# Kernel tuning notes

Measured on AMD Instinct MI355X. Metric: run time of the kernel, lower is better.

## Reference

```python
import jax, jax.numpy as jnp
import numpy as np

D_MODEL = 2048
D_HEAD = 128
NUM_HEADS = 16
D_KV_LATENT = 512
BATCH = 2
SEQ = 2048


def setup_inputs() -> dict:
    key = jax.random.key(0)
    ks = jax.random.split(key, 6)
    s = 0.02
    return {
        "x": jax.random.normal(ks[0], (BATCH, SEQ, D_MODEL), jnp.float32),
        "Wd": jax.random.normal(ks[1], (D_KV_LATENT, D_MODEL), jnp.float32) * s,
        "Wuk": jax.random.normal(ks[2], (NUM_HEADS * D_HEAD, D_KV_LATENT), jnp.float32) * s,
        "Wuv": jax.random.normal(ks[3], (NUM_HEADS * D_HEAD, D_KV_LATENT), jnp.float32) * s,
        "Wq": jax.random.normal(ks[4], (NUM_HEADS * D_HEAD, D_MODEL), jnp.float32) * s,
        "Wo": jax.random.normal(ks[5], (D_MODEL, NUM_HEADS * D_HEAD), jnp.float32) * s,
        "use_cache": 1,
    }


def _mla_cache_path(x, Wd, Wuk, Wuv, Wq, Wo):
    # Weight-absorbed MLA prefill from an empty cache (total_seq_len == seq_len).
    b, s, dm = x.shape
    h, dh, c = NUM_HEADS, D_HEAD, D_KV_LATENT
    # latents = downsample(x): [b, s, c]
    latents = jnp.einsum("bsm,cm->bsc", x, Wd)
    # absorbed weights: q_uk [h, dm, c], out_uv [h, dm, c]
    q_uk = jnp.einsum("hdm,hdc->hmc", Wq.reshape(h, dh, dm), Wuk.reshape(h, dh, c))
    out_uv = jnp.einsum("mhd,hdc->hmc", Wo.reshape(dm, h, dh), Wuv.reshape(h, dh, c))
    # query_part: [b, h, s, c]
    query_part = jnp.einsum("bsm,hmc->bhsc", x, q_uk)
    # value_part: [b, h, s, dm]
    value_part = jnp.einsum("hmc,btc->bhtm", out_uv, latents)
    # scores over latent dim: [b, h, s, s]
    scores = jnp.einsum("bhsc,btc->bhst", query_part, latents) / np.sqrt(dh).astype(np.float32)
    causal = jnp.triu(jnp.ones((s, s), dtype=bool), k=1)
    scores = jnp.where(causal, -jnp.inf, scores)
    attn = jax.nn.softmax(scores, axis=-1)
    # output already in model dim; sum contributions over heads
    out = jnp.einsum("bhst,bhtm->bsm", attn, value_part)
    return out


def reference(x, Wd, Wuk, Wuv, Wq, Wo, use_cache):
    # use_cache is a static Python int (1 -> weight-absorbed cache path)
    return _mla_cache_path(x, Wd, Wuk, Wuv, Wq, Wo)
```

## Files before the change

### kernel.cpp

```cpp
#include <hip/hip_runtime.h>
#include <hip/hip_bf16.h>

typedef __attribute__((ext_vector_type(8))) short short8x;
typedef __attribute__((ext_vector_type(4))) float f32x4;

__device__ __forceinline__ ushort f2bf(float f){
  union { __hip_bfloat16 b; ushort u; } cvt;
  cvt.b = __float2bfloat16(f);
  return cvt.u;
}

__global__ __launch_bounds__(256) void cvt_kernel(const float* __restrict__ in, ushort* __restrict__ out,
                                                  long n, float scale){
  long i = ((long)blockIdx.x * 256 + threadIdx.x) * 4;
  if (i >= n) return;
  float4 v = *(const float4*)(in + i);
  ushort4 o;
  o.x = f2bf(v.x * scale); o.y = f2bf(v.y * scale); o.z = f2bf(v.z * scale); o.w = f2bf(v.w * scale);
  *(ushort4*)(out + i) = o;
}

template<int OUTBF>
__global__ __launch_bounds__(256, 3)
void gemm_bt(const ushort* __restrict__ A, const ushort* __restrict__ BT, void* __restrict__ Cv,
             int M, int N, int K, int lda, int ldb, int ldc,
             long aZ, long bZ, long cZ, float scale)
{
  __shared__ __align__(16) ushort As[2][128 * 32];
  __shared__ __align__(16) ushort Bs[2][128 * 32];
  const int z = blockIdx.z;
  const ushort* Ab = A + (long)z * aZ;
  const ushort* Bb = BT + (long)z * bZ;
  const int tid = threadIdx.x, lane = tid & 63, w = tid >> 6;
  const int wm = w >> 1, wn = w & 1;
  const int lq = lane & 15, q4 = lane >> 4;

  int lin = blockIdx.x + gridDim.x * blockIdx.y;
  const int cpx = (gridDim.x * gridDim.y) >> 3;
  lin = (lin & 7) * cpx + (lin >> 3);
  const int bx = lin % gridDim.x, by = lin / gridDim.x;

  const long arow = (long)by * 128, brow = (long)bx * 128;
  const int lr = lane >> 2, lc = (lane & 3) * 8;

  const f32x4 z4 = {0.f, 0.f, 0.f, 0.f};
  f32x4 acc[4][4];
#pragma unroll
  for (int i = 0; i < 4; i++)
#pragma unroll
    for (int j = 0; j < 4; j++) acc[i][j] = z4;

  auto stage = [&](int buf, int k0){
#pragma unroll
    for (int is = 0; is < 2; ++is){
      const int rb = is * 64 + w * 16;
      const ushort* ga = Ab + (arow + rb + lr) * (long)lda + k0 + lc;
      const ushort* gb = Bb + (brow + rb + lr) * (long)ldb + k0 + lc;
      __builtin_amdgcn_global_load_lds((const __attribute__((address_space(1))) void*)ga,
                                       (__attribute__((address_space(3))) void*)&As[buf][rb * 32], 16, 0, 0);
      __builtin_amdgcn_global_load_lds((const __attribute__((address_space(1))) void*)gb,
                                       (__attribute__((address_space(3))) void*)&Bs[buf][rb * 32], 16, 0, 0);
    }
  };

  const int nk = K >> 5;
  stage(0, 0);
  for (int kt = 0; kt < nk; ++kt){
    __syncthreads();
    if (kt + 1 < nk) stage((kt + 1) & 1, (kt + 1) * 32);
    const int buf = kt & 1;
    short8x a[4], b[4];
#pragma unroll
    for (int i = 0; i < 4; i++){
      a[i] = *(const short8x*)&As[buf][(wm * 64 + i * 16 + lq) * 32 + q4 * 8];
      b[i] = *(const short8x*)&Bs[buf][(wn * 64 + i * 16 + lq) * 32 + q4 * 8];
    }
#pragma unroll
    for (int i = 0; i < 4; i++)
#pragma unroll
      for (int j = 0; j < 4; j++)
        acc[i][j] = __builtin_amdgcn_mfma_f32_16x16x32_bf16(a[i], b[j], acc[i][j], 0, 0, 0);
  }

  const long crowb = arow + wm * 64;
  const long ccolb = brow + wn * 64;
#pragma unroll
  for (int i = 0; i < 4; i++)
#pragma unroll
    for (int j = 0; j < 4; j++)
#pragma unroll
      for (int r = 0; r < 4; r++){
        const long row = crowb + i * 16 + q4 * 4 + r;
        const long col = ccolb + j * 16 + lq;
        const float v = acc[i][j][r] * scale;
        if (OUTBF) ((ushort*)Cv)[(long)z * cZ + row * ldc + col] = f2bf(v);
        else       ((float*)Cv)[(long)z * cZ + row * ldc + col] = v;
      }
}

__global__ __launch_bounds__(256, 1)
void flash12_kernel(const ushort* __restrict__ q, const ushort* __restrict__ k,
                    const ushort* __restrict__ vT, ushort* __restrict__ attnO)
{
  __shared__ __align__(16) ushort Kb[2][64 * 128];
  __shared__ __align__(16) ushort Vb[2][128 * 64];
  __shared__ __align__(16) ushort Pl[4][2][16][64];

  const int tid = threadIdx.x, lane = tid & 63, w = tid >> 6;
  const int lq = lane & 15, q4 = lane >> 4;

  const int i = blockIdx.x;
  const int pr = i >> 8;
  const int ii = i & 255;
  const int xcd = ii & 7;
  const int bh = xcd * 4 + ((ii >> 3) & 3);
  const int j = ii >> 5;
  const int strip = pr ? j : (15 - j);
  const int b = bh & 1, h = bh >> 1;

  const int nt = 2 * (strip + 1);
  const int wdiag = strip * 2 + (w >> 1);
  const int moff = (w & 1) * 32;

  const ushort* kb_ = k + (long)b * 2048 * 2048 + h * 128;
  const ushort* vb_ = vT + (long)h * 128 * 4096 + (long)b * 2048;

  const int krow0 = w * 4 + (lane >> 4);
  const int kg = (lane & 15) ^ (krow0 & 7);
  const ushort* kbase = kb_ + (long)krow0 * 2048 + kg * 8;
  const int kofs0 = w * 512;

  const int drow0 = w * 8 + (lane >> 3);
  const int vg = (lane & 7) ^ (drow0 & 7);
  const ushort* vbase = vb_ + (long)drow0 * 4096 + vg * 8;
  const int vofs0 = w * 512;

  auto stage = [&](int buf, int tt){
    const ushort* kp = kbase + (long)tt * 64 * 2048;
    const ushort* vp = vbase + (long)tt * 64;
#pragma unroll
    for (int is = 0; is < 4; ++is){
      __builtin_amdgcn_global_load_lds((const __attribute__((address_space(1))) void*)(kp + (long)is * 16 * 2048),
          (__attribute__((address_space(3))) void*)&Kb[buf][kofs0 + is * 2048], 16, 0, 0);
      __builtin_amdgcn_global_load_lds((const __attribute__((address_space(1))) void*)(vp + (long)is * 32 * 4096),
          (__attribute__((address_space(3))) void*)&Vb[buf][vofs0 + is * 2048], 16, 0, 0);
    }
  };

  const f32x4 z4 = {0.f, 0.f, 0.f, 0.f};

  const int qrow0 = strip * 128 + w * 32;
  const long qgbase = (long)b * 2048 + qrow0;

  short8x qf[2][4];
#pragma unroll
  for (int si = 0; si < 2; si++){
    const ushort* qp = q + (qgbase + si * 16 + lq) * 2560 + h * 128 + q4 * 8;
#pragma unroll
    for (int ks = 0; ks < 4; ks++) qf[si][ks] = *(const short8x*)(qp + ks * 32);
  }

  f32x4 oacc[8][2];
#pragma unroll
  for (int dt = 0; dt < 8; dt++){ oacc[dt][0] = z4; oacc[dt][1] = z4; }
  float dsum[2] = {0.f, 0.f};

  const int prx = lq & 7;

  stage(0, 0);
  stage(1, 1);

#pragma unroll 1
  for (int tt = 0; tt < nt; ++tt){
    if (tt == nt - 1) asm volatile("s_waitcnt vmcnt(0)" ::: "memory");
    else              asm volatile("s_waitcnt vmcnt(8)" ::: "memory");
    __syncthreads();
    const int cur = tt & 1;

    if (tt <= wdiag){
      const bool diag = (tt == wdiag);
#pragma unroll
      for (int ti = 0; ti < 4; ++ti){
        const int r = ti * 16 + lq;
        const int rb = r * 128;
        const int rx = r & 7;
        const short8x a0 = *(const short8x*)&Kb[cur][rb + (((q4) ^ rx) * 8)];
        const short8x a1 = *(const short8x*)&Kb[cur][rb + (((4 + q4) ^ rx) * 8)];
        const short8x a2 = *(const short8x*)&Kb[cur][rb + (((8 + q4) ^ rx) * 8)];
        const short8x a3 = *(const short8x*)&Kb[cur][rb + (((12 + q4) ^ rx) * 8)];
        const int cG = (ti * 2 + (q4 >> 1)) ^ prx;
        const int pco = cG * 8 + (q4 & 1) * 4;
#pragma unroll
        for (int si = 0; si < 2; ++si){
          f32x4 st = __builtin_amdgcn_mfma_f32_16x16x32_bf16(a0, qf[si][0], z4, 0, 0, 0);
          st = __builtin_amdgcn_mfma_f32_16x16x32_bf16(a1, qf[si][1], st, 0, 0, 0);
          st = __builtin_amdgcn_mfma_f32_16x16x32_bf16(a2, qf[si][2], st, 0, 0, 0);
          st = __builtin_amdgcn_mfma_f32_16x16x32_bf16(a3, qf[si][3], st, 0, 0, 0);
          ushort4 pb;
#pragma unroll
          for (int r4 = 0; r4 < 4; ++r4){
            const int tl = ti * 16 + q4 * 4 + r4;
            float p = exp2f(st[r4]);
            if (diag && tl > moff + si * 16 + lq) p = 0.f;
            dsum[si] += p;
            ((ushort*)&pb)[r4] = f2bf(p);
          }
          *(ushort4*)&Pl[w][si][lq][pco] = pb;
        }
      }
      asm volatile("s_waitcnt lgkmcnt(0)" ::: "memory");
      __builtin_amdgcn_sched_barrier(0);
      const short8x pf00 = *(const short8x*)&Pl[w][0][lq][(q4 ^ prx) * 8];
      const short8x pf01 = *(const short8x*)&Pl[w][0][lq][((4 + q4) ^ prx) * 8];
      const short8x pf10 = *(const short8x*)&Pl[w][1][lq][(q4 ^ prx) * 8];
      const short8x pf11 = *(const short8x*)&Pl[w][1][lq][((4 + q4) ^ prx) * 8];
      __builtin_amdgcn_sched_barrier(0);
#pragma unroll
      for (int dt = 0; dt < 8; ++dt){
        const int r = dt * 16 + lq;
        const int rb = r * 64;
        const int rx = lq & 7;
        const short8x av0 = *(const short8x*)&Vb[cur][rb + (((q4) ^ rx) * 8)];
        const short8x av1 = *(const short8x*)&Vb[cur][rb + (((4 + q4) ^ rx) * 8)];
        oacc[dt][0] = __builtin_amdgcn_mfma_f32_16x16x32_bf16(av0, pf00, oacc[dt][0], 0, 0, 0);
        oacc[dt][0] = __builtin_amdgcn_mfma_f32_16x16x32_bf16(av1, pf01, oacc[dt][0], 0, 0, 0);
        oacc[dt][1] = __builtin_amdgcn_mfma_f32_16x16x32_bf16(av0, pf10, oacc[dt][1], 0, 0, 0);
        oacc[dt][1] = __builtin_amdgcn_mfma_f32_16x16x32_bf16(av1, pf11, oacc[dt][1], 0, 0, 0);
      }
    }
    __syncthreads();
    if (tt + 2 < nt) stage(cur, tt + 2);
  }

  float inv[2];
#pragma unroll
  for (int si = 0; si < 2; ++si){
    float d = dsum[si];
    d += __shfl_xor(d, 16);
    d += __shfl_xor(d, 32);
    inv[si] = 1.f / d;
  }

#pragma unroll
  for (int dt = 0; dt < 8; dt++)
#pragma unroll
    for (int si = 0; si < 2; si++){
      ushort4 o;
      o.x = f2bf(oacc[dt][si][0] * inv[si]);
      o.y = f2bf(oacc[dt][si][1] * inv[si]);
      o.z = f2bf(oacc[dt][si][2] * inv[si]);
      o.w = f2bf(oacc[dt][si][3] * inv[si]);
      *(ushort4*)(attnO + (qgbase + si * 16 + lq) * 2048 + h * 128 + dt * 16 + q4 * 4) = o;
    }
}

extern "C" void kernel_launch(void* const* d_in, const int* in_sizes, int n_in,
                              void* d_out, int out_size, void* d_ws, size_t ws_size,
                              hipStream_t stream)
{
  const float* x   = (const float*)d_in[0];
  const float* Wd  = (const float*)d_in[1];
  const float* Wuk = (const float*)d_in[2];
  const float* Wuv = (const float*)d_in[3];
  const float* Wq  = (const float*)d_in[4];
  const float* Wo  = (const float*)d_in[5];
  float* out = (float*)d_out;
  ushort* ws = (ushort*)d_ws;

  ushort* xb    = ws + 0L;
  ushort* wqdb  = ws + 8388608L;
  ushort* wob   = ws + 13631488L;
  ushort* wukb  = ws + 17825792L;
  ushort* wuvb  = ws + 18874368L;
  ushort* qlat  = ws + 19922944L;
  ushort* kb    = ws + 30408704L;
  ushort* vTb   = ws + 38797312L;
  ushort* attnO = ws + 47185920L;

  const float QSCL = 0.12751744800f;

  cvt_kernel<<<8192, 256, 0, stream>>>(x,   xb,            8388608L, 1.0f);
  cvt_kernel<<<4096, 256, 0, stream>>>(Wq,  wqdb,          4194304L, QSCL);
  cvt_kernel<<<1024, 256, 0, stream>>>(Wd,  wqdb + 4194304L, 1048576L, 1.0f);
  cvt_kernel<<<4096, 256, 0, stream>>>(Wo,  wob,           4194304L, 1.0f);
  cvt_kernel<<<1024, 256, 0, stream>>>(Wuk, wukb,          1048576L, 1.0f);
  cvt_kernel<<<1024, 256, 0, stream>>>(Wuv, wuvb,          1048576L, 1.0f);

  gemm_bt<1><<<dim3(20, 32, 1), 256, 0, stream>>>(xb, wqdb, qlat, 4096, 2560, 2048,
      2048, 2048, 2560, 0L, 0L, 0L, 1.0f);
  gemm_bt<1><<<dim3(16, 32, 1), 256, 0, stream>>>(qlat + 2048, wukb, kb, 4096, 2048, 512,
      2560, 512, 2048, 0L, 0L, 0L, 1.0f);
  gemm_bt<1><<<dim3(32, 16, 1), 256, 0, stream>>>(wuvb, qlat + 2048, vTb, 2048, 4096, 512,
      512, 2560, 4096, 0L, 0L, 0L, 1.0f);
  flash12_kernel<<<512, 256, 0, stream>>>(qlat, kb, vTb, attnO);
  gemm_bt<0><<<dim3(16, 32, 1), 256, 0, stream>>>(attnO, wob, out, 4096, 2048, 2048,
      2048, 2048, 2048, 0L, 0L, 0L, 1.0f);
}
```

Before: 237.8 us.

## Replace 128x128 GEMM with 256x256 tile, swizzled LDS, two-stage prefetch

Rewrites the bf16 GEMM to use 256x256 output tiles with 512 threads, a K step of 64, XOR-swizzled LDS layout, and two buffers prefetched ahead with explicit vmcnt waits and wave priority hints. The aim is to raise operand reuse per LDS load and hide global-load latency behind MFMA work. All four projection GEMMs switch to it. The larger tiles cut the block count below the CU count and use a large LDS footprint, which can leave compute units idle, especially for the K=512 GEMMs.

```diff
diff --git a/kernel.cpp b/kernel.cpp
--- a/kernel.cpp
+++ b/kernel.cpp
@@ -21,71 +21,103 @@
 }
 
 template<int OUTBF>
-__global__ __launch_bounds__(256, 3)
-void gemm_bt(const ushort* __restrict__ A, const ushort* __restrict__ BT, void* __restrict__ Cv,
-             int M, int N, int K, int lda, int ldb, int ldc,
-             long aZ, long bZ, long cZ, float scale)
+__global__ __launch_bounds__(512, 1)
+void gemm256(const ushort* __restrict__ A, const ushort* __restrict__ BT, void* __restrict__ Cv,
+             int K, int lda, int ldb, int ldc, float scale)
 {
-  __shared__ __align__(16) ushort As[2][128 * 32];
-  __shared__ __align__(16) ushort Bs[2][128 * 32];
-  const int z = blockIdx.z;
-  const ushort* Ab = A + (long)z * aZ;
-  const ushort* Bb = BT + (long)z * bZ;
+  __shared__ __align__(16) ushort As[2][256 * 64];
+  __shared__ __align__(16) ushort Bs[2][256 * 64];
   const int tid = threadIdx.x, lane = tid & 63, w = tid >> 6;
-  const int wm = w >> 1, wn = w & 1;
   const int lq = lane & 15, q4 = lane >> 4;
+  const int wm = w >> 2, wn = w & 3;
 
   int lin = blockIdx.x + gridDim.x * blockIdx.y;
   const int cpx = (gridDim.x * gridDim.y) >> 3;
   lin = (lin & 7) * cpx + (lin >> 3);
   const int bx = lin % gridDim.x, by = lin / gridDim.x;
-
-  const long arow = (long)by * 128, brow = (long)bx * 128;
-  const int lr = lane >> 2, lc = (lane & 3) * 8;
+  const long arow = (long)by * 256, brow = (long)bx * 256;
+
+  const int srow = tid >> 3;
+  const int sg = (tid & 7) ^ (srow & 7);
+  const ushort* Abase = A + (arow + srow) * (long)lda + sg * 8;
+  const ushort* Bbase = BT + (brow + srow) * (long)ldb + sg * 8;
+  const int dof = w * 512;
+
+  auto stage = [&](int buf, int kt){
+    const long kc = (long)kt * 64;
+#pragma unroll
+    for (int s = 0; s < 4; ++s){
+      __builtin_amdgcn_global_load_lds(
+          (const __attribute__((address_space(1))) void*)(Abase + (long)(s * 64) * lda + kc),
+          (__attribute__((address_space(3))) void*)&As[buf][s * 4096 + dof], 16, 0, 0);
+      __builtin_amdgcn_global_load_lds(
+          (const __attribute__((address_space(1))) void*)(Bbase + (long)(s * 64) * ldb + kc),
+          (__attribute__((address_space(3))) void*)&Bs[buf][s * 4096 + dof], 16, 0, 0);
+    }
+  };
 
   const f32x4 z4 = {0.f, 0.f, 0.f, 0.f};
-  f32x4 acc[4][4];
-#pragma unroll
-  for (int i = 0; i < 4; i++)
+  f32x4 acc[8][4];
+#pragma unroll
+  for (int i = 0; i < 8; i++)
 #pragma unroll
     for (int j = 0; j < 4; j++) acc[i][j] = z4;
 
-  auto stage = [&](int buf, int k0){
-#pragma unroll
-    for (int is = 0; is < 2; ++is){
-      const int rb = is * 64 + w * 16;
-      const ushort* ga = Ab + (arow + rb + lr) * (long)lda + k0 + lc;
-      const ushort* gb = Bb + (brow + rb + lr) * (long)ldb + k0 + lc;
-      __builtin_amdgcn_global_load_lds((const __attribute__((address_space(1))) void*)ga,
-                                       (__attribute__((address_space(3))) void*)&As[buf][rb * 32], 16, 0, 0);
-      __builtin_amdgcn_global_load_lds((const __attribute__((address_space(1))) void*)gb,
-                                       (__attribute__((address_space(3))) void*)&Bs[buf][rb * 32], 16, 0, 0);
-    }
-  };
-
-  const int nk = K >> 5;
+  const int rx = lq & 7;
+  const int arb = wm * 128;
+  const int brb = wn * 64;
+
+  const int nk = K >> 6;
   stage(0, 0);
+  stage(1, 1);
+
+#pragma unroll 1
   for (int kt = 0; kt < nk; ++kt){
+    if (kt == nk - 1) asm volatile("s_waitcnt vmcnt(0)" ::: "memory");
+    else              asm volatile("s_waitcnt vmcnt(8)" ::: "memory");
     __syncthreads();
-    if (kt + 1 < nk) stage((kt + 1) & 1, (kt + 1) * 32);
     const int buf = kt & 1;
-    short8x a[4], b[4];
-#pragma unroll
-    for (int i = 0; i < 4; i++){
-      a[i] = *(const short8x*)&As[buf][(wm * 64 + i * 16 + lq) * 32 + q4 * 8];
-      b[i] = *(const short8x*)&Bs[buf][(wn * 64 + i * 16 + lq) * 32 + q4 * 8];
-    }
-#pragma unroll
-    for (int i = 0; i < 4; i++)
-#pragma unroll
-      for (int j = 0; j < 4; j++)
-        acc[i][j] = __builtin_amdgcn_mfma_f32_16x16x32_bf16(a[i], b[j], acc[i][j], 0, 0, 0);
+
+#pragma unroll
+    for (int q = 0; q < 4; ++q){
+      const int mi = q & 1, nj = q >> 1;
+      short8x af[4][2], bf[2][2];
+#pragma unroll
+      for (int i2 = 0; i2 < 4; ++i2){
+        const int R = arb + (mi * 4 + i2) * 16 + lq;
+#pragma unroll
+        for (int kk = 0; kk < 2; ++kk)
+          af[i2][kk] = *(const short8x*)&As[buf][R * 64 + (((kk * 4 + q4) ^ rx) * 8)];
+      }
+#pragma unroll
+      for (int j2 = 0; j2 < 2; ++j2){
+        const int R = brb + (nj * 2 + j2) * 16 + lq;
+#pragma unroll
+        for (int kk = 0; kk < 2; ++kk)
+          bf[j2][kk] = *(const short8x*)&Bs[buf][R * 64 + (((kk * 4 + q4) ^ rx) * 8)];
+      }
+      asm volatile("s_waitcnt lgkmcnt(0)" ::: "memory");
+      __builtin_amdgcn_sched_barrier(0);
+      __builtin_amdgcn_s_setprio(1);
+#pragma unroll
+      for (int kk = 0; kk < 2; ++kk)
+#pragma unroll
+        for (int i2 = 0; i2 < 4; ++i2)
+#pragma unroll
+          for (int j2 = 0; j2 < 2; ++j2)
+            acc[mi * 4 + i2][nj * 2 + j2] =
+                __builtin_amdgcn_mfma_f32_16x16x32_bf16(af[i2][kk], bf[j2][kk],
+                                                        acc[mi * 4 + i2][nj * 2 + j2], 0, 0, 0);
+      __builtin_amdgcn_s_setprio(0);
+    }
+    __syncthreads();
+    if (kt + 2 < nk) stage(buf, kt + 2);
   }
 
-  const long crowb = arow + wm * 64;
+  const long crowb = arow + wm * 128;
   const long ccolb = brow + wn * 64;
 #pragma unroll
-  for (int i = 0; i < 4; i++)
+  for (int i = 0; i < 8; i++)
 #pragma unroll
     for (int j = 0; j < 4; j++)
 #pragma unroll
@@ -93,8 +125,8 @@
         const long row = crowb + i * 16 + q4 * 4 + r;
         const long col = ccolb + j * 16 + lq;
         const float v = acc[i][j][r] * scale;
-        if (OUTBF) ((ushort*)Cv)[(long)z * cZ + row * ldc + col] = f2bf(v);
-        else       ((float*)Cv)[(long)z * cZ + row * ldc + col] = v;
+        if (OUTBF) ((ushort*)Cv)[row * ldc + col] = f2bf(v);
+        else       ((float*)Cv)[row * ldc + col] = v;
       }
 }
 
@@ -183,11 +215,11 @@
       for (int ti = 0; ti < 4; ++ti){
         const int r = ti * 16 + lq;
         const int rb = r * 128;
-        const int rx = r & 7;
-        const short8x a0 = *(const short8x*)&Kb[cur][rb + (((q4) ^ rx) * 8)];
-        const short8x a1 = *(const short8x*)&Kb[cur][rb + (((4 + q4) ^ rx) * 8)];
-        const short8x a2 = *(const short8x*)&Kb[cur][rb + (((8 + q4) ^ rx) * 8)];
-        const short8x a3 = *(const short8x*)&Kb[cur][rb + (((12 + q4) ^ rx) * 8)];
+        const int rxk = r & 7;
+        const short8x a0 = *(const short8x*)&Kb[cur][rb + (((q4) ^ rxk) * 8)];
+        const short8x a1 = *(const short8x*)&Kb[cur][rb + (((4 + q4) ^ rxk) * 8)];
+        const short8x a2 = *(const short8x*)&Kb[cur][rb + (((8 + q4) ^ rxk) * 8)];
+        const short8x a3 = *(const short8x*)&Kb[cur][rb + (((12 + q4) ^ rxk) * 8)];
         const int cG = (ti * 2 + (q4 >> 1)) ^ prx;
         const int pco = cG * 8 + (q4 & 1) * 4;
 #pragma unroll
@@ -219,9 +251,9 @@
       for (int dt = 0; dt < 8; ++dt){
         const int r = dt * 16 + lq;
         const int rb = r * 64;
-        const int rx = lq & 7;
-        const short8x av0 = *(const short8x*)&Vb[cur][rb + (((q4) ^ rx) * 8)];
-        const short8x av1 = *(const short8x*)&Vb[cur][rb + (((4 + q4) ^ rx) * 8)];
+        const int rxv = lq & 7;
+        const short8x av0 = *(const short8x*)&Vb[cur][rb + (((q4) ^ rxv) * 8)];
+        const short8x av1 = *(const short8x*)&Vb[cur][rb + (((4 + q4) ^ rxv) * 8)];
         oacc[dt][0] = __builtin_amdgcn_mfma_f32_16x16x32_bf16(av0, pf00, oacc[dt][0], 0, 0, 0);
         oacc[dt][0] = __builtin_amdgcn_mfma_f32_16x16x32_bf16(av1, pf01, oacc[dt][0], 0, 0, 0);
         oacc[dt][1] = __builtin_amdgcn_mfma_f32_16x16x32_bf16(av0, pf10, oacc[dt][1], 0, 0, 0);
@@ -286,13 +318,9 @@
   cvt_kernel<<<1024, 256, 0, stream>>>(Wuk, wukb,          1048576L, 1.0f);
   cvt_kernel<<<1024, 256, 0, stream>>>(Wuv, wuvb,          1048576L, 1.0f);
 
-  gemm_bt<1><<<dim3(20, 32, 1), 256, 0, stream>>>(xb, wqdb, qlat, 4096, 2560, 2048,
-      2048, 2048, 2560, 0L, 0L, 0L, 1.0f);
-  gemm_bt<1><<<dim3(16, 32, 1), 256, 0, stream>>>(qlat + 2048, wukb, kb, 4096, 2048, 512,
-      2560, 512, 2048, 0L, 0L, 0L, 1.0f);
-  gemm_bt<1><<<dim3(32, 16, 1), 256, 0, stream>>>(wuvb, qlat + 2048, vTb, 2048, 4096, 512,
-      512, 2560, 4096, 0L, 0L, 0L, 1.0f);
+  gemm256<1><<<dim3(10, 16), 512, 0, stream>>>(xb, wqdb, qlat, 2048, 2048, 2048, 2560, 1.0f);
+  gemm256<1><<<dim3(8, 16), 512, 0, stream>>>(qlat + 2048, wukb, kb, 512, 2560, 512, 2048, 1.0f);
+  gemm256<1><<<dim3(16, 8), 512, 0, stream>>>(wuvb, qlat + 2048, vTb, 512, 512, 2560, 4096, 1.0f);
   flash12_kernel<<<512, 256, 0, stream>>>(qlat, kb, vTb, attnO);
-  gemm_bt<0><<<dim3(16, 32, 1), 256, 0, stream>>>(attnO, wob, out, 4096, 2048, 2048,
-      2048, 2048, 2048, 0L, 0L, 0L, 1.0f);
-}
+  gemm256<0><<<dim3(8, 16), 512, 0, stream>>>(attnO, wob, out, 2048, 2048, 2048, 2048, 1.0f);
+}
```

New measurement: 295.7 us. 1.24x slower.

## Halve flash attention tile sizes to raise occupancy and block count

Applied to the files above, without the earlier changes.

The attention kernel now processes 64-row query strips with 16 rows per wave and 32-key tiles, instead of 128-row strips and 64-key tiles. This cuts LDS and registers per block so four blocks can share a CU, and launches 1024 blocks with a reworked strip and XCD mapping for causal load balance. In exchange, each block issues twice as many tile iterations and barriers, K/V reuse per load is lower, and the V and P LDS layouts drop their swizzle, which may add bank conflicts.

```diff
diff --git a/kernel.cpp b/kernel.cpp
--- a/kernel.cpp
+++ b/kernel.cpp
@@ -98,29 +98,27 @@
       }
 }
 
-__global__ __launch_bounds__(256, 1)
-void flash12_kernel(const ushort* __restrict__ q, const ushort* __restrict__ k,
+__global__ __launch_bounds__(256, 4)
+void flash13_kernel(const ushort* __restrict__ q, const ushort* __restrict__ k,
                     const ushort* __restrict__ vT, ushort* __restrict__ attnO)
 {
-  __shared__ __align__(16) ushort Kb[2][64 * 128];
-  __shared__ __align__(16) ushort Vb[2][128 * 64];
-  __shared__ __align__(16) ushort Pl[4][2][16][64];
+  __shared__ __align__(16) ushort Kb[2][32 * 128];
+  __shared__ __align__(16) ushort Vb[2][128 * 32];
+  __shared__ __align__(16) ushort Pl[4][16][40];
 
   const int tid = threadIdx.x, lane = tid & 63, w = tid >> 6;
   const int lq = lane & 15, q4 = lane >> 4;
 
-  const int i = blockIdx.x;
-  const int pr = i >> 8;
-  const int ii = i & 255;
-  const int xcd = ii & 7;
-  const int bh = xcd * 4 + ((ii >> 3) & 3);
-  const int j = ii >> 5;
-  const int strip = pr ? j : (15 - j);
+  const int blk = blockIdx.x;
+  const int bh = (blk & 7) * 4 + ((blk >> 3) & 3);
+  const int g = blk >> 5;
+  const int u = (g & 7) * 4 + (g >> 3);
+  const int strip = (u & 1) ? (u >> 1) : (31 - (u >> 1));
   const int b = bh & 1, h = bh >> 1;
 
-  const int nt = 2 * (strip + 1);
+  const int nt = 2 * strip + 2;
   const int wdiag = strip * 2 + (w >> 1);
-  const int moff = (w & 1) * 32;
+  const int moff = (w & 1) * 16;
 
   const ushort* kb_ = k + (long)b * 2048 * 2048 + h * 128;
   const ushort* vb_ = vT + (long)h * 128 * 4096 + (long)b * 2048;
@@ -128,44 +126,38 @@
   const int krow0 = w * 4 + (lane >> 4);
   const int kg = (lane & 15) ^ (krow0 & 7);
   const ushort* kbase = kb_ + (long)krow0 * 2048 + kg * 8;
-  const int kofs0 = w * 512;
-
-  const int drow0 = w * 8 + (lane >> 3);
-  const int vg = (lane & 7) ^ (drow0 & 7);
-  const ushort* vbase = vb_ + (long)drow0 * 4096 + vg * 8;
-  const int vofs0 = w * 512;
+
+  const int drow0 = w * 16 + (lane >> 2);
+  const ushort* vbase = vb_ + (long)drow0 * 4096 + (lane & 3) * 8;
 
   auto stage = [&](int buf, int tt){
-    const ushort* kp = kbase + (long)tt * 64 * 2048;
-    const ushort* vp = vbase + (long)tt * 64;
-#pragma unroll
-    for (int is = 0; is < 4; ++is){
+    const ushort* kp = kbase + (long)tt * 32 * 2048;
+    const ushort* vp = vbase + (long)tt * 32;
+#pragma unroll
+    for (int is = 0; is < 2; ++is){
       __builtin_amdgcn_global_load_lds((const __attribute__((address_space(1))) void*)(kp + (long)is * 16 * 2048),
-          (__attribute__((address_space(3))) void*)&Kb[buf][kofs0 + is * 2048], 16, 0, 0);
-      __builtin_amdgcn_global_load_lds((const __attribute__((address_space(1))) void*)(vp + (long)is * 32 * 4096),
-          (__attribute__((address_space(3))) void*)&Vb[buf][vofs0 + is * 2048], 16, 0, 0);
+          (__attribute__((address_space(3))) void*)&Kb[buf][w * 512 + is * 2048], 16, 0, 0);
+      __builtin_amdgcn_global_load_lds((const __attribute__((address_space(1))) void*)(vp + (long)is * 64 * 4096),
+          (__attribute__((address_space(3))) void*)&Vb[buf][w * 512 + is * 2048], 16, 0, 0);
     }
   };
 
   const f32x4 z4 = {0.f, 0.f, 0.f, 0.f};
 
-  const int qrow0 = strip * 128 + w * 32;
+  const int qrow0 = strip * 64 + w * 16;
   const long qgbase = (long)b * 2048 + qrow0;
 
-  short8x qf[2][4];
-#pragma unroll
-  for (int si = 0; si < 2; si++){
-    const ushort* qp = q + (qgbase + si * 16 + lq) * 2560 + h * 128 + q4 * 8;
-#pragma unroll
-    for (int ks = 0; ks < 4; ks++) qf[si][ks] = *(const short8x*)(qp + ks * 32);
-  }
-
-  f32x4 oacc[8][2];
-#pragma unroll
-  for (int dt = 0; dt < 8; dt++){ oacc[dt][0] = z4; oacc[dt][1] = z4; }
-  float dsum[2] = {0.f, 0.f};
-
-  const int prx = lq & 7;
+  short8x qf[4];
+  {
+    const ushort* qp = q + (qgbase + lq) * 2560 + h * 128 + q4 * 8;
+#pragma unroll
+    for (int ks = 0; ks < 4; ks++) qf[ks] = *(const short8x*)(qp + ks * 32);
+  }
+
+  f32x4 oacc[8];
+#pragma unroll
+  for (int dt = 0; dt < 8; dt++) oacc[dt] = z4;
+  float dsum = 0.f;
 
   stage(0, 0);
   stage(1, 1);
@@ -173,85 +165,63 @@
 #pragma unroll 1
   for (int tt = 0; tt < nt; ++tt){
     if (tt == nt - 1) asm volatile("s_waitcnt vmcnt(0)" ::: "memory");
-    else              asm volatile("s_waitcnt vmcnt(8)" ::: "memory");
+    else              asm volatile("s_waitcnt vmcnt(4)" ::: "memory");
     __syncthreads();
     const int cur = tt & 1;
 
     if (tt <= wdiag){
       const bool diag = (tt == wdiag);
 #pragma unroll
-      for (int ti = 0; ti < 4; ++ti){
+      for (int ti = 0; ti < 2; ++ti){
         const int r = ti * 16 + lq;
         const int rb = r * 128;
-        const int rx = r & 7;
+        const int rx = lq & 7;
         const short8x a0 = *(const short8x*)&Kb[cur][rb + (((q4) ^ rx) * 8)];
         const short8x a1 = *(const short8x*)&Kb[cur][rb + (((4 + q4) ^ rx) * 8)];
         const short8x a2 = *(const short8x*)&Kb[cur][rb + (((8 + q4) ^ rx) * 8)];
         const short8x a3 = *(const short8x*)&Kb[cur][rb + (((12 + q4) ^ rx) * 8)];
-        const int cG = (ti * 2 + (q4 >> 1)) ^ prx;
-        const int pco = cG * 8 + (q4 & 1) * 4;
-#pragma unroll
-        for (int si = 0; si < 2; ++si){
-          f32x4 st = __builtin_amdgcn_mfma_f32_16x16x32_bf16(a0, qf[si][0], z4, 0, 0, 0);
-          st = __builtin_amdgcn_mfma_f32_16x16x32_bf16(a1, qf[si][1], st, 0, 0, 0);
-          st = __builtin_amdgcn_mfma_f32_16x16x32_bf16(a2, qf[si][2], st, 0, 0, 0);
-          st = __builtin_amdgcn_mfma_f32_16x16x32_bf16(a3, qf[si][3], st, 0, 0, 0);
-          ushort4 pb;
-#pragma unroll
-          for (int r4 = 0; r4 < 4; ++r4){
-            const int tl = ti * 16 + q4 * 4 + r4;
-            float p = exp2f(st[r4]);
-            if (diag && tl > moff + si * 16 + lq) p = 0.f;
-            dsum[si] += p;
-            ((ushort*)&pb)[r4] = f2bf(p);
-          }
-          *(ushort4*)&Pl[w][si][lq][pco] = pb;
+        f32x4 st = __builtin_amdgcn_mfma_f32_16x16x32_bf16(a0, qf[0], z4, 0, 0, 0);
+        st = __builtin_amdgcn_mfma_f32_16x16x32_bf16(a1, qf[1], st, 0, 0, 0);
+        st = __builtin_amdgcn_mfma_f32_16x16x32_bf16(a2, qf[2], st, 0, 0, 0);
+        st = __builtin_amdgcn_mfma_f32_16x16x32_bf16(a3, qf[3], st, 0, 0, 0);
+        ushort4 pb;
+#pragma unroll
+        for (int r4 = 0; r4 < 4; ++r4){
+          const int tl = ti * 16 + q4 * 4 + r4;
+          float p = exp2f(st[r4]);
+          if (diag && tl > moff + lq) p = 0.f;
+          dsum += p;
+          ((ushort*)&pb)[r4] = f2bf(p);
         }
+        *(ushort4*)&Pl[w][lq][ti * 16 + q4 * 4] = pb;
       }
       asm volatile("s_waitcnt lgkmcnt(0)" ::: "memory");
       __builtin_amdgcn_sched_barrier(0);
-      const short8x pf00 = *(const short8x*)&Pl[w][0][lq][(q4 ^ prx) * 8];
-      const short8x pf01 = *(const short8x*)&Pl[w][0][lq][((4 + q4) ^ prx) * 8];
-      const short8x pf10 = *(const short8x*)&Pl[w][1][lq][(q4 ^ prx) * 8];
-      const short8x pf11 = *(const short8x*)&Pl[w][1][lq][((4 + q4) ^ prx) * 8];
+      const short8x pf = *(const short8x*)&Pl[w][lq][q4 * 8];
       __builtin_amdgcn_sched_barrier(0);
 #pragma unroll
       for (int dt = 0; dt < 8; ++dt){
-        const int r = dt * 16 + lq;
-        const int rb = r * 64;
-        const int rx = lq & 7;
-        const short8x av0 = *(const short8x*)&Vb[cur][rb + (((q4) ^ rx) * 8)];
-        const short8x av1 = *(const short8x*)&Vb[cur][rb + (((4 + q4) ^ rx) * 8)];
-        oacc[dt][0] = __builtin_amdgcn_mfma_f32_16x16x32_bf16(av0, pf00, oacc[dt][0], 0, 0, 0);
-        oacc[dt][0] = __builtin_amdgcn_mfma_f32_16x16x32_bf16(av1, pf01, oacc[dt][0], 0, 0, 0);
-        oacc[dt][1] = __builtin_amdgcn_mfma_f32_16x16x32_bf16(av0, pf10, oacc[dt][1], 0, 0, 0);
-        oacc[dt][1] = __builtin_amdgcn_mfma_f32_16x16x32_bf16(av1, pf11, oacc[dt][1], 0, 0, 0);
+        const short8x av = *(const short8x*)&Vb[cur][(dt * 16 + lq) * 32 + q4 * 8];
+        oacc[dt] = __builtin_amdgcn_mfma_f32_16x16x32_bf16(av, pf, oacc[dt], 0, 0, 0);
       }
     }
     __syncthreads();
     if (tt + 2 < nt) stage(cur, tt + 2);
   }
 
-  float inv[2];
-#pragma unroll
-  for (int si = 0; si < 2; ++si){
-    float d = dsum[si];
-    d += __shfl_xor(d, 16);
-    d += __shfl_xor(d, 32);
-    inv[si] = 1.f / d;
-  }
-
-#pragma unroll
-  for (int dt = 0; dt < 8; dt++)
-#pragma unroll
-    for (int si = 0; si < 2; si++){
-      ushort4 o;
-      o.x = f2bf(oacc[dt][si][0] * inv[si]);
-      o.y = f2bf(oacc[dt][si][1] * inv[si]);
-      o.z = f2bf(oacc[dt][si][2] * inv[si]);
-      o.w = f2bf(oacc[dt][si][3] * inv[si]);
-      *(ushort4*)(attnO + (qgbase + si * 16 + lq) * 2048 + h * 128 + dt * 16 + q4 * 4) = o;
-    }
+  dsum += __shfl_xor(dsum, 16);
+  dsum += __shfl_xor(dsum, 32);
+  const float inv = 1.f / dsum;
+
+#pragma unroll
+  for (int dt = 0; dt < 8; dt++){
+    ushort4 o;
+    o.x = f2bf(oacc[dt][0] * inv);
+    o.y = f2bf(oacc[dt][1] * inv);
+    o.z = f2bf(oacc[dt][2] * inv);
+    o.w = f2bf(oacc[dt][3] * inv);
+    *(ushort4*)(attnO + (qgbase + lq) * 2048 + h * 128 + dt * 16 + q4 * 4) = o;
+  }
 }
 
 extern "C" void kernel_launch(void* const* d_in, const int* in_sizes, int n_in,
@@ -292,7 +262,7 @@
       2560, 512, 2048, 0L, 0L, 0L, 1.0f);
   gemm_bt<1><<<dim3(32, 16, 1), 256, 0, stream>>>(wuvb, qlat + 2048, vTb, 2048, 4096, 512,
       512, 2560, 4096, 0L, 0L, 0L, 1.0f);
-  flash12_kernel<<<512, 256, 0, stream>>>(qlat, kb, vTb, attnO);
+  flash13_kernel<<<1024, 256, 0, stream>>>(qlat, kb, vTb, attnO);
   gemm_bt<0><<<dim3(16, 32, 1), 256, 0, stream>>>(attnO, wob, out, 4096, 2048, 2048,
       2048, 2048, 2048, 0L, 0L, 0L, 1.0f);
 }
```

Result: no change. 236.5 us (-0.5%).
